# Kernel tuning notes

Measured on AMD Instinct MI355X. Metric: run time of the kernel, lower is better.

Reference implementation:

```python
import jax, jax.numpy as jnp
import numpy as np

B, T, C = 4, 4096, 1024
H, G = 16, 8
HS = C // H      # head size = 64
GT = T // G      # group_t = 512
KAPX = 1         # k_apx


def causal_attn(q, k, v):
    # q,k,v: [..., L, d]; causal softmax attention within last two dims
    d = q.shape[-1]
    s = jnp.einsum('...qd,...kd->...qk', q, k) / jnp.sqrt(jnp.asarray(d, q.dtype))
    mask = jnp.tril(jnp.ones((s.shape[-2], s.shape[-1]), dtype=bool))
    s = jnp.where(mask, s, jnp.asarray(-1e30, s.dtype))
    return jnp.einsum('...qk,...kd->...qd', jax.nn.softmax(s, axis=-1), v)


def apply_rope(x, cos, sin):
    # x: [B,H,T,HS]; cos/sin: [T,HS//2]; interleaved (even,odd) complex pairs
    xr = x.reshape(x.shape[:-1] + (HS // 2, 2))
    r, i = xr[..., 0], xr[..., 1]
    c = cos[None, None]
    s = sin[None, None]
    return jnp.stack([r * c - i * s, r * s + i * c], axis=-1).reshape(x.shape)


def setup_inputs() -> dict:
    key = jax.random.key(0)
    k1, k2, k3, k4, k5, k6 = jax.random.split(key, 6)
    x = jax.random.normal(k1, (B, T, C), jnp.float32)
    lim = 1.0 / np.sqrt(C)
    Wqkv = jax.random.uniform(k2, (C, 3 * C), jnp.float32, -lim, lim)
    Wo = jax.random.uniform(k3, (C, C), jnp.float32, -lim, lim)
    # init_() uses std = 1/sqrt(last_dim) = 1/sqrt(k_apx) = 1
    q_proj = jax.random.uniform(k4, (GT, KAPX), jnp.float32, -1.0, 1.0)
    k_proj = jax.random.uniform(k5, (GT, KAPX), jnp.float32, -1.0, 1.0)
    v_proj = jax.random.uniform(k6, (GT, KAPX), jnp.float32, -1.0, 1.0)
    inv = 1.0 / (10000.0 ** (np.arange(0, HS, 2) / HS))
    ang = np.outer(np.arange(T), inv)
    freqs_cos = jnp.asarray(np.cos(ang), jnp.float32)
    freqs_sin = jnp.asarray(np.sin(ang), jnp.float32)
    return dict(x=x, Wqkv=Wqkv, Wo=Wo, q_proj=q_proj, k_proj=k_proj,
                v_proj=v_proj, freqs_cos=freqs_cos, freqs_sin=freqs_sin)


def reference(x, Wqkv, Wo, q_proj, k_proj, v_proj, freqs_cos, freqs_sin):
    q, k, v = jnp.split(x @ Wqkv, 3, axis=-1)          # each [B,T,C]
    q = q.reshape(B, T, H, HS).transpose(0, 2, 1, 3)    # [B,H,T,HS]
    k = k.reshape(B, T, H, HS).transpose(0, 2, 1, 3)
    q = apply_rope(q, freqs_cos, freqs_sin)
    k = apply_rope(k, freqs_cos, freqs_sin)
    # torch .view on contiguous [B,H,T,HS]: raw row-major reinterpretation
    q = q.reshape(B, G, GT, H, HS).transpose(0, 3, 1, 2, 4)  # [B,H,G,GT,HS]
    k = k.reshape(B, G, GT, H, HS).transpose(0, 3, 1, 2, 4)
    v = v.reshape(B, G, GT, H, HS).transpose(0, 3, 1, 2, 4)  # v viewed from [B,T,C]
    # its_time branch: learned time-pooling of all but last group
    qb = jnp.einsum('bhgtc,tk->bhgkc', q[:, :, :-1], q_proj)  # [B,H,G-1,1,HS]
    kb = jnp.einsum('bhgtc,tk->bhgkc', k[:, :, :-1], k_proj)
    vb = jnp.einsum('bhgtc,tk->bhgkc', v[:, :, :-1], v_proj)
    o = causal_attn(q, k, v)          # block-local causal attention [B,H,G,GT,HS]
    vb = causal_attn(qb, kb, vb)      # compressed block attention [B,H,G-1,1,HS]
    o = o.reshape(B, H, G * GT, HS).transpose(0, 2, 1, 3).reshape(B, T, C)
    out = o @ Wo                       # dropout=0 (eval)
    return (out, qb, kb, vb)
```

## Files before the change

kernel.cpp:

```cpp
#include <hip/hip_runtime.h>


typedef float  float4_t  __attribute__((ext_vector_type(4)));
typedef short  bfrag     __attribute__((ext_vector_type(8)));
typedef unsigned short ushort8 __attribute__((ext_vector_type(8)));

#define MFMA_BF16(A, B, C) __builtin_amdgcn_mfma_f32_16x16x32_bf16((A), (B), (C), 0, 0, 0)

__device__ __forceinline__ unsigned short f2bf(float f) {
  union { float f; unsigned u; } v; v.f = f;
  return (unsigned short)((v.u + 0x7FFFu + ((v.u >> 16) & 1u)) >> 16);
}
__device__ __forceinline__ float bf2f(unsigned short h) {
  union { unsigned u; float f; } v; v.u = ((unsigned)h) << 16; return v.f;
}
__device__ __forceinline__ void async16(const void* g, void* l) {
  __builtin_amdgcn_global_load_lds(
      (const __attribute__((address_space(1))) unsigned int*)(unsigned long long)g,
      (__attribute__((address_space(3))) unsigned int*)(unsigned long long)l,
      16, 0, 0);
}

__global__ __launch_bounds__(256) void cvt_kernel(const float* __restrict__ in,
                                                  unsigned short* __restrict__ out, int n8) {
  int i = blockIdx.x * 256 + threadIdx.x;
  if (i >= n8) return;
  const float4_t* p = (const float4_t*)in + (size_t)i * 2;
  float4_t a = p[0], c = p[1];
  ushort8 r;
  r[0] = f2bf(a[0]); r[1] = f2bf(a[1]); r[2] = f2bf(a[2]); r[3] = f2bf(a[3]);
  r[4] = f2bf(c[0]); r[5] = f2bf(c[1]); r[6] = f2bf(c[2]); r[7] = f2bf(c[3]);
  *((ushort8*)out + i) = r;
}

__global__ void transpose_cvt_kernel(const float* __restrict__ in,
                                     unsigned short* __restrict__ out, int R, int C) {
  __shared__ float t[32][33];
  int bc = blockIdx.x * 32, br = blockIdx.y * 32;
  int x = threadIdx.x, y = threadIdx.y;
  for (int i = 0; i < 32; i += 8) t[y + i][x] = in[(size_t)(br + y + i) * C + bc + x];
  __syncthreads();
  for (int i = 0; i < 32; i += 8) out[(size_t)(bc + y + i) * R + br + x] = f2bf(t[x][y + i]);
}

__global__ void transpose2_f32_kernel(const float* __restrict__ a,
                                      const float* __restrict__ b,
                                      float* __restrict__ oa, float* __restrict__ ob_,
                                      int R, int C) {
  const float* in = blockIdx.z ? b : a;
  float* out = blockIdx.z ? ob_ : oa;
  __shared__ float t[32][33];
  int bc = blockIdx.x * 32, br = blockIdx.y * 32;
  int x = threadIdx.x, y = threadIdx.y;
  for (int i = 0; i < 32; i += 8) t[y + i][x] = in[(size_t)(br + y + i) * C + bc + x];
  __syncthreads();
  for (int i = 0; i < 32; i += 8) out[(size_t)(bc + y + i) * R + br + x] = t[x][y + i];
}

__device__ __forceinline__ void gemm_core(const unsigned short* __restrict__ A,
                                          const unsigned short* __restrict__ BT,
                                          int bm0, int bn0, int K,
                                          unsigned short* As, unsigned short* Bs,
                                          float4_t acc[4][4]) {
  int tid = threadIdx.x, w = tid >> 6;
  int lane = tid & 63, quad = lane >> 4, l16 = lane & 15;
  int wm = w >> 1, wn = w & 1;
  int rr = tid >> 2, xx = tid & 3;
  for (int k0 = 0; k0 < K; k0 += 32) {
    __syncthreads();
    {
      int r0 = rr,       s0 = xx ^ ((r0 >> 1) & 3);
      int r1 = rr + 64,  s1 = xx ^ ((r1 >> 1) & 3);
      async16(&A [(size_t)(bm0 + r0) * K + k0 + s0 * 8], &As[(size_t)(w * 64) * 8]);
      async16(&A [(size_t)(bm0 + r1) * K + k0 + s1 * 8], &As[(size_t)(256 + w * 64) * 8]);
      async16(&BT[(size_t)(bn0 + r0) * K + k0 + s0 * 8], &Bs[(size_t)(w * 64) * 8]);
      async16(&BT[(size_t)(bn0 + r1) * K + k0 + s1 * 8], &Bs[(size_t)(256 + w * 64) * 8]);
    }
    __syncthreads();
    bfrag af[4], bf_[4];
    for (int i = 0; i < 4; ++i) {
      int rm = wm * 64 + i * 16 + l16;
      af[i]  = *(const bfrag*)&As[(size_t)(rm * 4 + (quad ^ ((rm >> 1) & 3))) * 8];
      int rn = wn * 64 + i * 16 + l16;
      bf_[i] = *(const bfrag*)&Bs[(size_t)(rn * 4 + (quad ^ ((rn >> 1) & 3))) * 8];
    }
    for (int i = 0; i < 4; ++i)
      for (int j = 0; j < 4; ++j)
        acc[i][j] = MFMA_BF16(af[i], bf_[j], acc[i][j]);
  }
}

__global__ __launch_bounds__(256) void gemm1_kernel(const unsigned short* __restrict__ xb,
    const unsigned short* __restrict__ wqkvT,
    const float* __restrict__ fcT, const float* __restrict__ fsT,
    unsigned short* __restrict__ qkv) {
  __shared__ __align__(16) unsigned short As[128 * 32];
  __shared__ __align__(16) unsigned short Bs[128 * 32];
  __shared__ __align__(16) float Es[4 * 1088];
  float4_t acc[4][4];
  for (int i = 0; i < 4; ++i) for (int j = 0; j < 4; ++j)
    acc[i][j] = (float4_t){0.f, 0.f, 0.f, 0.f};
  int bn0 = blockIdx.x * 128, bm0 = blockIdx.y * 128;
  gemm_core(xb, wqkvT, bm0, bn0, 1024, As, Bs, acc);

  int tid = threadIdx.x, w = tid >> 6, lane = tid & 63, quad = lane >> 4, l16 = lane & 15;
  int wm = w >> 1, wn = w & 1;

  for (int i = 0; i < 4; ++i) {
    int t0 = (bm0 + wm * 64 + i * 16 + quad * 4) & 4095;
    for (int j = 0; j < 4; ++j) {
      int gcol = bn0 + wn * 64 + j * 16 + l16;
      if (gcol < 2048) {
        int ci = (gcol & 63) >> 1;
        const float4_t c4 = *(const float4_t*)&fcT[(size_t)ci * 4096 + t0];
        const float4_t s4 = *(const float4_t*)&fsT[(size_t)ci * 4096 + t0];
        for (int r = 0; r < 4; ++r) {
          float val = acc[i][j][r];
          float partner = __shfl_xor(val, 1);
          float c = c4[r], s = s4[r];
          acc[i][j][r] = (gcol & 1) ? fmaf(partner, s, val * c)
                                    : fmaf(-partner, s, val * c);
        }
      }
    }
  }

  float* slice = &Es[w * 1088];
  for (int i = 0; i < 4; ++i) {
    for (int j = 0; j < 4; ++j)
      for (int r = 0; r < 4; ++r)
        slice[(quad * 4 + r) * 68 + j * 16 + l16] = acc[i][j][r];
    for (int m = 0; m < 2; ++m) {
      int rl = m * 8 + (lane >> 3);
      int cb = (lane & 7) * 8;
      const float* rp = &slice[rl * 68 + cb];
      ushort8 outv;
      outv[0] = f2bf(rp[0]); outv[1] = f2bf(rp[1]);
      outv[2] = f2bf(rp[2]); outv[3] = f2bf(rp[3]);
      outv[4] = f2bf(rp[4]); outv[5] = f2bf(rp[5]);
      outv[6] = f2bf(rp[6]); outv[7] = f2bf(rp[7]);
      int grow = bm0 + wm * 64 + i * 16 + rl;
      int gcol = bn0 + wn * 64 + cb;
      *(ushort8*)&qkv[(size_t)grow * 3072 + gcol] = outv;
    }
  }
}

__global__ __launch_bounds__(256) void gemm2_kernel(const unsigned short* __restrict__ ob,
    const unsigned short* __restrict__ woT, float* __restrict__ outp) {
  __shared__ __align__(16) unsigned short As[128 * 32];
  __shared__ __align__(16) unsigned short Bs[128 * 32];
  float4_t acc[4][4];
  for (int i = 0; i < 4; ++i) for (int j = 0; j < 4; ++j)
    acc[i][j] = (float4_t){0.f, 0.f, 0.f, 0.f};
  int bn0 = blockIdx.x * 128, bm0 = blockIdx.y * 128;
  gemm_core(ob, woT, bm0, bn0, 1024, As, Bs, acc);
  int tid = threadIdx.x, w = tid >> 6, lane = tid & 63, quad = lane >> 4, l16 = lane & 15;
  int wm = w >> 1, wn = w & 1;
  for (int i = 0; i < 4; ++i)
    for (int j = 0; j < 4; ++j)
      for (int r = 0; r < 4; ++r)
        outp[(size_t)(bm0 + wm * 64 + i * 16 + quad * 4 + r) * 1024 +
             bn0 + wn * 64 + j * 16 + l16] = acc[i][j][r];
}

__global__ __launch_bounds__(512) void attn_kernel(const unsigned short* __restrict__ qkv,
    unsigned short* __restrict__ ob) {
  __shared__ __align__(16) unsigned short Ks[128 * 64];
  __shared__ __align__(16) unsigned short VTs[64 * 136];
  __shared__ __align__(16) unsigned short Ps[8 * 16 * 136];
  int bx = blockIdx.x;
  int qt2 = bx & 3, g = (bx >> 2) & 7, h = (bx >> 5) & 15, b = bx >> 9;
  int tid = threadIdx.x, w = tid >> 6, lane = tid & 63, quad = lane >> 4, l16 = lane & 15;

  const unsigned short* QKb = qkv + ((size_t)b * 4096 + h) * 3072 + g * 128;
  const unsigned short* Vb  = qkv + ((size_t)(b * 4096 + g * 512)) * 3072 + 2048 + h * 64;

  int qrow = qt2 * 128 + w * 16 + l16;
  const unsigned short* Qr = QKb + ((size_t)((qrow & 255) << 4)) * 3072 + (qrow >> 8) * 64;
  bfrag qf0 = *(const bfrag*)&Qr[quad * 8];
  bfrag qf1 = *(const bfrag*)&Qr[32 + quad * 8];

  float4_t acc[4];
#pragma unroll
  for (int i = 0; i < 4; ++i) acc[i] = (float4_t){0.f, 0.f, 0.f, 0.f};
  float m_i[4] = {-1e30f, -1e30f, -1e30f, -1e30f};
  float l_i[4] = {0.f, 0.f, 0.f, 0.f};

  int skey = tid >> 3, sx = tid & 7, ss = sx ^ (skey & 7);
  int kp = tid & 63, hsg = tid >> 6;
  unsigned short* Pw = &Ps[w * 2176];
  int ntiles = qt2 + 1;

  for (int kt = 0; kt < ntiles; ++kt) {
    __syncthreads();
#pragma unroll
    for (int c = 0; c < 2; ++c) {
      int krow = kt * 128 + 64 * c + skey;
      async16(&QKb[((size_t)((krow & 255) << 4)) * 3072 + (krow >> 8) * 64 + 1024 + ss * 8],
              &Ks[(size_t)(c * 512 + w * 64) * 8]);
    }
    {
      const unsigned short* vp0 = Vb + (size_t)(kt * 128 + kp * 2) * 3072 + hsg * 8;
      ushort8 va0 = *(const ushort8*)vp0;
      ushort8 vb0 = *(const ushort8*)(vp0 + 3072);
#pragma unroll
      for (int e = 0; e < 8; ++e)
        *(unsigned*)&VTs[(size_t)(hsg * 8 + e) * 136 + kp * 2] =
            (unsigned)va0[e] | ((unsigned)vb0[e] << 16);
    }
    __syncthreads();

    float4_t s[8];
#pragma unroll
    for (int c = 0; c < 8; ++c) s[c] = (float4_t){0.f, 0.f, 0.f, 0.f};
    {
      int sl0 = l16 * 8 + (quad ^ (l16 & 7));
      int sl1 = l16 * 8 + ((4 + quad) ^ (l16 & 7));
#pragma unroll
      for (int c = 0; c < 8; ++c) {
        s[c] = MFMA_BF16(qf0, *(const bfrag*)&Ks[(size_t)(sl0 + 128 * c) * 8], s[c]);
        s[c] = MFMA_BF16(qf1, *(const bfrag*)&Ks[(size_t)(sl1 + 128 * c) * 8], s[c]);
      }
    }

    int qa = qt2 * 128 + w * 16 + quad * 4;
    int kb0 = kt * 128 + l16;
#pragma unroll
    for (int r = 0; r < 4; ++r) {
      float vv[8];
#pragma unroll
      for (int c = 0; c < 8; ++c) {
        vv[c] = s[c][r] * 0.125f;
        if (kb0 + 16 * c > qa + r) vv[c] = -1e30f;
      }
      float tm = fmaxf(fmaxf(fmaxf(vv[0], vv[1]), fmaxf(vv[2], vv[3])),
                       fmaxf(fmaxf(vv[4], vv[5]), fmaxf(vv[6], vv[7])));
      tm = fmaxf(tm, __shfl_xor(tm, 1));
      tm = fmaxf(tm, __shfl_xor(tm, 2));
      tm = fmaxf(tm, __shfl_xor(tm, 4));
      tm = fmaxf(tm, __shfl_xor(tm, 8));
      float nm = fmaxf(m_i[r], tm);
      float alpha = __expf(m_i[r] - nm);
      m_i[r] = nm;
      float p[8], rs = 0.f;
#pragma unroll
      for (int c = 0; c < 8; ++c) { p[c] = __expf(vv[c] - nm); rs += p[c]; }
      rs += __shfl_xor(rs, 1);
      rs += __shfl_xor(rs, 2);
      rs += __shfl_xor(rs, 4);
      rs += __shfl_xor(rs, 8);
      l_i[r] = l_i[r] * alpha + rs;
      acc[0][r] *= alpha; acc[1][r] *= alpha; acc[2][r] *= alpha; acc[3][r] *= alpha;
      int pr = (quad * 4 + r) * 136 + l16;
#pragma unroll
      for (int c = 0; c < 8; ++c) Pw[pr + 16 * c] = f2bf(p[c]);
    }
    bfrag pf[4];
#pragma unroll
    for (int c = 0; c < 4; ++c)
      pf[c] = *(const bfrag*)&Pw[(size_t)l16 * 136 + 32 * c + quad * 8];
#pragma unroll
    for (int ht = 0; ht < 4; ++ht) {
#pragma unroll
      for (int c = 0; c < 4; ++c) {
        bfrag vf = *(const bfrag*)&VTs[(size_t)(ht * 16 + l16) * 136 + 32 * c + quad * 8];
        acc[ht] = MFMA_BF16(pf[c], vf, acc[ht]);
      }
    }
  }

  int orow = b * 4096 + g * 512 + qt2 * 128 + w * 16 + quad * 4;
#pragma unroll
  for (int ht = 0; ht < 4; ++ht)
#pragma unroll
    for (int r = 0; r < 4; ++r)
      ob[(size_t)(orow + r) * 1024 + h * 64 + ht * 16 + l16] = f2bf(acc[ht][r] / l_i[r]);
}

__global__ __launch_bounds__(1024) void pools_kernel(const unsigned short* __restrict__ qkv,
    const float* __restrict__ qp, const float* __restrict__ kp,
    const float* __restrict__ vp, float* __restrict__ outp) {
  __shared__ float red[3][16][64];
  int g = blockIdx.x, h = blockIdx.y, b = blockIdx.z;
  int hs = threadIdx.x & 63, tc = threadIdx.x >> 6;
  const unsigned short* qb_ = qkv + ((size_t)b * 4096 + h) * 3072 + g * 128 + hs;
  const unsigned short* vb_ = qkv + ((size_t)(b * 4096 + g * 512)) * 3072 + 2048 + h * 64 + hs;
  float aq = 0.f, ak = 0.f, av = 0.f;
  int t0 = tc * 32;
  for (int t = t0; t < t0 + 32; ++t) {
    size_t qoff = ((size_t)((t & 255) << 4)) * 3072 + (t >> 8) * 64;
    aq = fmaf(bf2f(qb_[qoff]), qp[t], aq);
    ak = fmaf(bf2f(qb_[qoff + 1024]), kp[t], ak);
    av = fmaf(bf2f(vb_[(size_t)t * 3072]), vp[t], av);
  }
  red[0][tc][hs] = aq;
  red[1][tc][hs] = ak;
  red[2][tc][hs] = av;
  __syncthreads();
  if (tc < 3) {
    float a = 0.f;
    for (int c = 0; c < 16; ++c) a += red[tc][c][hs];
    size_t oi = (((size_t)b * 16 + h) * 7 + g) * 64 + hs;
    size_t off = (tc == 0) ? 0 : (tc == 1) ? 28672 : 57344;
    outp[16777216 + off + oi] = a;
  }
}

extern "C" void kernel_launch(void* const* d_in, const int* in_sizes, int n_in,
                              void* d_out, int out_size, void* d_ws, size_t ws_size,
                              hipStream_t stream) {
  (void)in_sizes; (void)n_in; (void)out_size; (void)ws_size;
  const float* x    = (const float*)d_in[0];
  const float* Wqkv = (const float*)d_in[1];
  const float* Wo   = (const float*)d_in[2];
  const float* qp   = (const float*)d_in[3];
  const float* kp   = (const float*)d_in[4];
  const float* vp   = (const float*)d_in[5];
  const float* fc   = (const float*)d_in[6];
  const float* fs   = (const float*)d_in[7];
  float* outp = (float*)d_out;

  char* ws = (char*)d_ws;
  unsigned short* xb    = (unsigned short*)(ws);
  unsigned short* wqkvT = (unsigned short*)(ws + 33554432);
  unsigned short* woT   = (unsigned short*)(ws + 39845888);
  unsigned short* qkv   = (unsigned short*)(ws + 41943040);
  unsigned short* ob    = xb;

  float* fcT = outp;
  float* fsT = outp + 131072;

  cvt_kernel<<<8192, 256, 0, stream>>>(x, xb, 2097152);
  transpose_cvt_kernel<<<dim3(96, 32), dim3(32, 8), 0, stream>>>(Wqkv, wqkvT, 1024, 3072);
  transpose_cvt_kernel<<<dim3(32, 32), dim3(32, 8), 0, stream>>>(Wo, woT, 1024, 1024);
  transpose2_f32_kernel<<<dim3(1, 128, 2), dim3(32, 8), 0, stream>>>(fc, fs, fcT, fsT, 4096, 32);
  gemm1_kernel<<<dim3(24, 128), 256, 0, stream>>>(xb, wqkvT, fcT, fsT, qkv);
  attn_kernel<<<2048, 512, 0, stream>>>(qkv, ob);
  pools_kernel<<<dim3(7, 16, 4), 1024, 0, stream>>>(qkv, qp, kp, vp, outp);
  gemm2_kernel<<<dim3(8, 128), 256, 0, stream>>>(ob, woT, outp);
}
```

Measured before the change: 484.8 us.

## Prefetch next K/V tile into registers during softmax and PV compute

Replaces the per-iteration async global-to-LDS K load and synchronous V load with a register-staged software pipeline. The next tile's K and V are loaded into registers right after the QK^T MFMAs, overlapping global latency with softmax and PV work, then written to LDS after a barrier. This hides memory latency at the cost of extra VGPRs, which may reduce occupancy, and replaces direct-to-LDS loads with register round-trips.

```diff
diff --git a/kernel.cpp b/kernel.cpp
--- a/kernel.cpp
+++ b/kernel.cpp
@@ -192,23 +192,24 @@
   unsigned short* Pw = &Ps[w * 2176];
   int ntiles = qt2 + 1;
 
+  ushort8 kreg0, kreg1, vreg0, vreg1;
+
+  {
+    int krow0 = skey, krow1 = 64 + skey;
+    kreg0 = *(const ushort8*)&QKb[((size_t)((krow0 & 255) << 4)) * 3072 + (krow0 >> 8) * 64 + 1024 + ss * 8];
+    kreg1 = *(const ushort8*)&QKb[((size_t)((krow1 & 255) << 4)) * 3072 + (krow1 >> 8) * 64 + 1024 + ss * 8];
+    const unsigned short* vp0 = Vb + (size_t)(kp * 2) * 3072 + hsg * 8;
+    vreg0 = *(const ushort8*)vp0;
+    vreg1 = *(const ushort8*)(vp0 + 3072);
+    *(ushort8*)&Ks[(size_t)(tid) * 8]       = kreg0;
+    *(ushort8*)&Ks[(size_t)(512 + tid) * 8] = kreg1;
+#pragma unroll
+    for (int e = 0; e < 8; ++e)
+      *(unsigned*)&VTs[(size_t)(hsg * 8 + e) * 136 + kp * 2] =
+          (unsigned)vreg0[e] | ((unsigned)vreg1[e] << 16);
+  }
+
   for (int kt = 0; kt < ntiles; ++kt) {
-    __syncthreads();
-#pragma unroll
-    for (int c = 0; c < 2; ++c) {
-      int krow = kt * 128 + 64 * c + skey;
-      async16(&QKb[((size_t)((krow & 255) << 4)) * 3072 + (krow >> 8) * 64 + 1024 + ss * 8],
-              &Ks[(size_t)(c * 512 + w * 64) * 8]);
-    }
-    {
-      const unsigned short* vp0 = Vb + (size_t)(kt * 128 + kp * 2) * 3072 + hsg * 8;
-      ushort8 va0 = *(const ushort8*)vp0;
-      ushort8 vb0 = *(const ushort8*)(vp0 + 3072);
-#pragma unroll
-      for (int e = 0; e < 8; ++e)
-        *(unsigned*)&VTs[(size_t)(hsg * 8 + e) * 136 + kp * 2] =
-            (unsigned)va0[e] | ((unsigned)vb0[e] << 16);
-    }
     __syncthreads();
 
     float4_t s[8];
@@ -222,6 +223,17 @@
         s[c] = MFMA_BF16(qf0, *(const bfrag*)&Ks[(size_t)(sl0 + 128 * c) * 8], s[c]);
         s[c] = MFMA_BF16(qf1, *(const bfrag*)&Ks[(size_t)(sl1 + 128 * c) * 8], s[c]);
       }
+    }
+
+    bool more = (kt + 1 < ntiles);
+    if (more) {
+      int kb = (kt + 1) * 128;
+      int krow0 = kb + skey, krow1 = kb + 64 + skey;
+      kreg0 = *(const ushort8*)&QKb[((size_t)((krow0 & 255) << 4)) * 3072 + (krow0 >> 8) * 64 + 1024 + ss * 8];
+      kreg1 = *(const ushort8*)&QKb[((size_t)((krow1 & 255) << 4)) * 3072 + (krow1 >> 8) * 64 + 1024 + ss * 8];
+      const unsigned short* vp0 = Vb + (size_t)(kb + kp * 2) * 3072 + hsg * 8;
+      vreg0 = *(const ushort8*)vp0;
+      vreg1 = *(const ushort8*)(vp0 + 3072);
     }
 
     int qa = qt2 * 128 + w * 16 + quad * 4;
@@ -267,6 +279,16 @@
         bfrag vf = *(const bfrag*)&VTs[(size_t)(ht * 16 + l16) * 136 + 32 * c + quad * 8];
         acc[ht] = MFMA_BF16(pf[c], vf, acc[ht]);
       }
+    }
+
+    __syncthreads();
+    if (more) {
+      *(ushort8*)&Ks[(size_t)(tid) * 8]       = kreg0;
+      *(ushort8*)&Ks[(size_t)(512 + tid) * 8] = kreg1;
+#pragma unroll
+      for (int e = 0; e < 8; ++e)
+        *(unsigned*)&VTs[(size_t)(hsg * 8 + e) * 136 + kp * 2] =
+            (unsigned)vreg0[e] | ((unsigned)vreg1[e] << 16);
     }
   }
 
```

New measurement: 483.2 us. No clear change (-0.3%).
